# Optimization experiments

Hardware: AMD Instinct MI355X
Metric: run time of the kernel (lower is better)

## Reference

```python
import jax, jax.numpy as jnp
import numpy as np
import math

S, B, D = 2048, 8, 256
HEADS = 8
DPROJ = 128
DFF = 1024
DH = DPROJ // HEADS  # 16


def _layernorm(x, g, b, eps=1e-5):
    mu = jnp.mean(x, axis=-1, keepdims=True)
    var = jnp.mean((x - mu) ** 2, axis=-1, keepdims=True)
    return (x - mu) * jax.lax.rsqrt(var + eps) * g + b


def setup_inputs() -> dict:
    key = jax.random.key(0)
    ks = jax.random.split(key, 16)
    s = 0.02
    return {
        "src": jax.random.normal(ks[0], (S, B, D), dtype=jnp.float32),
        "Wq": jax.random.normal(ks[1], (D, DPROJ), dtype=jnp.float32) * s,
        "bq": jnp.zeros((DPROJ,), dtype=jnp.float32),
        "Wk": jax.random.normal(ks[2], (D, DPROJ), dtype=jnp.float32) * s,
        "bk": jnp.zeros((DPROJ,), dtype=jnp.float32),
        "Wv": jax.random.normal(ks[3], (D, DPROJ), dtype=jnp.float32) * s,
        "bv": jnp.zeros((DPROJ,), dtype=jnp.float32),
        "Wo": jax.random.normal(ks[4], (DPROJ, D), dtype=jnp.float32) * s,
        "ln1_g": jnp.ones((D,), dtype=jnp.float32),
        "ln1_b": jnp.zeros((D,), dtype=jnp.float32),
        "W1": jax.random.normal(ks[5], (D, DFF), dtype=jnp.float32) * s,
        "b1": jnp.zeros((DFF,), dtype=jnp.float32),
        "W2": jax.random.normal(ks[6], (DFF, D), dtype=jnp.float32) * s,
        "b2": jnp.zeros((D,), dtype=jnp.float32),
        "ln2_g": jnp.ones((D,), dtype=jnp.float32),
        "ln2_b": jnp.zeros((D,), dtype=jnp.float32),
    }


def reference(src, Wq, bq, Wk, bk, Wv, bv, Wo, ln1_g, ln1_b, W1, b1, W2, b2, ln2_g, ln2_b):
    # src: (S, B, D)
    q = src @ Wq + bq  # (S, B, DPROJ)
    k = src @ Wk + bk
    v = src @ Wv + bv

    # _reshape_to_batches: (S, B, h*dh) -> (S, B*h, dh), then sdpa moves batch first
    def split_heads(x):
        return jnp.transpose(x.reshape(S, B * HEADS, DH), (1, 0, 2))  # (B*h, S, dh)

    qh, kh, vh = split_heads(q), split_heads(k), split_heads(v)
    scores = jnp.einsum('bid,bjd->bij', qh, kh) / math.sqrt(DH)  # (B*h, S, S)
    attn = jax.nn.softmax(scores, axis=-1)
    ctx = jnp.einsum('bij,bjd->bid', attn, vh)  # (B*h, S, dh)

    # _reshape_from_batches: (B*h, S, dh) -> (S, B, DPROJ)
    ctx = jnp.transpose(ctx, (1, 0, 2)).reshape(S, B, DPROJ)
    y = ctx @ Wo  # (S, B, D), no bias

    x = _layernorm(src + y, ln1_g, ln1_b)
    ffn = jax.nn.relu(x @ W1 + b1) @ W2 + b2
    return _layernorm(x + ffn, ln2_g, ln2_b)
```

## Files before the change

### kernel.cpp

```cpp
#include <hip/hip_runtime.h>
#include <math.h>

#define SLEN 2048
#define BATCH 8
#define DMODEL 256
#define HEADS 8
#define DPROJ 128
#define DFF 1024
#define DH 16
#define MROWS (SLEN*BATCH)

typedef unsigned short u16;
typedef unsigned int u32;
typedef __attribute__((ext_vector_type(8))) short short8;
typedef __attribute__((ext_vector_type(4))) float f32x4;
typedef __attribute__((ext_vector_type(16))) float f32x16;
typedef __attribute__((ext_vector_type(4))) unsigned short u16x4;

__device__ __forceinline__ u16 f2bf(float x) {
    union { float f; u32 u; } v; v.f = x;
    u32 r = v.u + 0x7FFFu + ((v.u >> 16) & 1u);
    return (u16)(r >> 16);
}
__device__ __forceinline__ float bf2f(u16 h) {
    union { u32 u; float f; } v; v.u = ((u32)h) << 16;
    return v.f;
}
__device__ __forceinline__ float fexp2(float x) { return __builtin_amdgcn_exp2f(x); }
__device__ __forceinline__ u32 pack_bf(float lo, float hi) {
    union { float f; u32 u; } a, b; a.f = lo; b.f = hi;
    return __builtin_amdgcn_perm(b.u, a.u, 0x07060302u);
}
__device__ __forceinline__ void gld16(const u16* g, u16* l) {
    __builtin_amdgcn_global_load_lds(
        (const __attribute__((address_space(1))) void*)g,
        (__attribute__((address_space(3))) void*)l, 16, 0, 0);
}

__global__ void prep_kernel(const float* __restrict__ src, u16* __restrict__ srcb,
                            const float* __restrict__ Wq, const float* __restrict__ Wk,
                            const float* __restrict__ Wv, const float* __restrict__ Wo,
                            const float* __restrict__ W1, const float* __restrict__ W2,
                            u16* __restrict__ WqT, u16* __restrict__ WkT,
                            u16* __restrict__ WvT, u16* __restrict__ WoT,
                            u16* __restrict__ W1T, u16* __restrict__ W2T) {
    if (blockIdx.x < 4096) {
        int idx = (blockIdx.x * 256 + threadIdx.x) * 4;
        float4 v = *(const float4*)(src + idx);
        u16x4 o;
        o.x = f2bf(v.x); o.y = f2bf(v.y); o.z = f2bf(v.z); o.w = f2bf(v.w);
        *(u16x4*)(srcb + idx) = o;
        return;
    }
    int i = (blockIdx.x - 4096) * 256 + threadIdx.x;
    if (i < 32768) {
        int n = i >> 8, k = i & 255;
        WqT[i] = f2bf(Wq[k * 128 + n]);
    } else if (i < 65536) {
        int j = i - 32768; int n = j >> 8, k = j & 255;
        WkT[j] = f2bf(Wk[k * 128 + n]);
    } else if (i < 98304) {
        int j = i - 65536; int n = j >> 8, k = j & 255;
        WvT[j] = f2bf(Wv[k * 128 + n]);
    } else if (i < 131072) {
        int j = i - 98304; int n = j >> 7, k = j & 127;
        WoT[j] = f2bf(Wo[k * 256 + n]);
    } else if (i < 393216) {
        int j = i - 131072; int n = j >> 8, k = j & 255;
        W1T[j] = f2bf(W1[k * 1024 + n]);
    } else if (i < 655360) {
        int j = i - 393216; int n = j >> 10, k = j & 1023;
        W2T[j] = f2bf(W2[k * 256 + n]);
    }
}

template<int BN, bool RELU, bool HAS_BIAS, bool OUT_BF16>
__global__ void mfma_gemm(const u16* __restrict__ A, const u16* __restrict__ BT,
                          const float* __restrict__ bias, void* __restrict__ Cout,
                          int M, int N, int K) {
    constexpr int NJ = BN / 32;
    __shared__ __align__(16) u16 As[128 * 32];
    __shared__ __align__(16) u16 Bs[BN * 32];
    const int tid = threadIdx.x;
    const int row0 = blockIdx.x * 128;
    const int col0 = blockIdx.y * BN;
    const int w = tid >> 6, l = tid & 63;
    const int wr = (w & 1) * 64, wc = (w >> 1) * (BN / 2);
    const int lcol = l & 15, lrow = (l >> 4) * 4, g = l >> 4;
    const int sl = l >> 2;
    const int swc = ((l & 3) ^ (sl & 3)) * 8;
    const int fsw = (g ^ (lcol & 3)) * 8;

    const u16* Ag0 = A + (size_t)(row0 + 16 * w + sl) * K + swc;
    const u16* Ag1 = Ag0 + (size_t)64 * K;
    const u16* Bg0 = BT + (size_t)(col0 + 16 * w + sl) * K + swc;
    const u16* Bg1 = Bg0 + (size_t)64 * K;
    u16* lA0 = As + (16 * w) * 32;
    u16* lA1 = As + (16 * w + 64) * 32;
    u16* lB0 = Bs + (16 * w) * 32;
    u16* lB1 = Bs + (16 * w + 64) * 32;

    f32x4 acc[4][NJ] = {};
    for (int k0 = 0; k0 < K; k0 += 32) {
        gld16(Ag0 + k0, lA0);
        gld16(Ag1 + k0, lA1);
        gld16(Bg0 + k0, lB0);
        if (BN == 128) gld16(Bg1 + k0, lB1);
        __syncthreads();
        short8 af[4], bf[NJ];
        #pragma unroll
        for (int i = 0; i < 4; ++i)
            af[i] = *(const short8*)(As + (wr + i * 16 + lcol) * 32 + fsw);
        #pragma unroll
        for (int j = 0; j < NJ; ++j)
            bf[j] = *(const short8*)(Bs + (wc + j * 16 + lcol) * 32 + fsw);
        #pragma unroll
        for (int i = 0; i < 4; ++i)
            #pragma unroll
            for (int j = 0; j < NJ; ++j)
                acc[i][j] = __builtin_amdgcn_mfma_f32_16x16x32_bf16(
                    af[i], bf[j], acc[i][j], 0, 0, 0);
        __syncthreads();
    }
    float bv[NJ];
    #pragma unroll
    for (int j = 0; j < NJ; ++j)
        bv[j] = HAS_BIAS ? bias[col0 + wc + j * 16 + lcol] : 0.f;
    #pragma unroll
    for (int i = 0; i < 4; ++i) {
        #pragma unroll
        for (int r = 0; r < 4; ++r) {
            size_t grow = row0 + wr + i * 16 + lrow + r;
            #pragma unroll
            for (int j = 0; j < NJ; ++j) {
                int gcol = col0 + wc + j * 16 + lcol;
                float c = acc[i][j][r] + bv[j];
                if (RELU) c = fmaxf(c, 0.f);
                if (OUT_BF16) ((u16*)Cout)[grow * N + gcol] = f2bf(c);
                else          ((float*)Cout)[grow * N + gcol] = c;
            }
        }
    }
}

__global__ void qkv_mfma(const u16* __restrict__ A,
                         const u16* __restrict__ WqT, const u16* __restrict__ WkT,
                         const u16* __restrict__ WvT,
                         const float* __restrict__ bq, const float* __restrict__ bk,
                         const float* __restrict__ bv,
                         u16* __restrict__ qhp, u16* __restrict__ khp,
                         u16* __restrict__ vhb) {
    const int which = blockIdx.z;
    const u16* BT   = which == 0 ? WqT : (which == 1 ? WkT : WvT);
    const float* bs = which == 0 ? bq : (which == 1 ? bk : bv);
    u16* outp       = which == 0 ? qhp : (which == 1 ? khp : vhb);
    const float scale = which == 0 ? 0.25f * 1.44269504f : 1.0f;
    __shared__ __align__(16) u16 As[128 * 32];
    __shared__ __align__(16) u16 Bs[128 * 32];
    const int tid = threadIdx.x;
    const int row0 = blockIdx.x * 128;
    const int w = tid >> 6, l = tid & 63;
    const int wr = (w & 1) * 64, wc = (w >> 1) * 64;
    const int lcol = l & 15, lrow = (l >> 4) * 4, g = l >> 4;
    const int sl = l >> 2;
    const int swc = ((l & 3) ^ (sl & 3)) * 8;
    const int fsw = (g ^ (lcol & 3)) * 8;

    const u16* Ag0 = A + (size_t)(row0 + 16 * w + sl) * DMODEL + swc;
    const u16* Ag1 = Ag0 + (size_t)64 * DMODEL;
    const u16* Bg0 = BT + (size_t)(16 * w + sl) * DMODEL + swc;
    const u16* Bg1 = Bg0 + (size_t)64 * DMODEL;
    u16* lA0 = As + (16 * w) * 32;
    u16* lA1 = As + (16 * w + 64) * 32;
    u16* lB0 = Bs + (16 * w) * 32;
    u16* lB1 = Bs + (16 * w + 64) * 32;

    f32x4 acc[4][4] = {};
    for (int k0 = 0; k0 < DMODEL; k0 += 32) {
        gld16(Ag0 + k0, lA0);
        gld16(Ag1 + k0, lA1);
        gld16(Bg0 + k0, lB0);
        gld16(Bg1 + k0, lB1);
        __syncthreads();
        short8 af[4], bf[4];
        #pragma unroll
        for (int i = 0; i < 4; ++i)
            af[i] = *(const short8*)(As + (wr + i * 16 + lcol) * 32 + fsw);
        #pragma unroll
        for (int j = 0; j < 4; ++j)
            bf[j] = *(const short8*)(Bs + (wc + j * 16 + lcol) * 32 + fsw);
        #pragma unroll
        for (int i = 0; i < 4; ++i)
            #pragma unroll
            for (int j = 0; j < 4; ++j)
                acc[i][j] = __builtin_amdgcn_mfma_f32_16x16x32_bf16(
                    af[i], bf[j], acc[i][j], 0, 0, 0);
        __syncthreads();
    }
    #pragma unroll
    for (int i = 0; i < 4; ++i) {
        #pragma unroll
        for (int r = 0; r < 4; ++r) {
            int grow = row0 + wr + i * 16 + lrow + r;
            int b = grow & 7, s = grow >> 3;
            #pragma unroll
            for (int j = 0; j < 4; ++j) {
                int gcol = wc + j * 16 + lcol;
                int h = gcol >> 4, d = gcol & 15;
                float c = acc[i][j][r] + bs[gcol];
                outp[((size_t)(b * 8 + h) * SLEN + s) * 16 + d] = f2bf(c * scale);
            }
        }
    }
}

__global__ void transpose_v(const u16* __restrict__ vhb, u16* __restrict__ va) {
    __shared__ u16 T[128 * 24];
    const int bh = blockIdx.y;
    const int c0 = blockIdx.x * 128;
    const int t = threadIdx.x;
    {
        int key = t >> 1, half = t & 1;
        *(uint4*)(T + key * 24 + half * 8) =
            *(const uint4*)(vhb + ((size_t)bh * SLEN + c0 + key) * 16 + half * 8);
    }
    __syncthreads();
    int d = t >> 4, k8 = (t & 15) * 8;
    u16x4 o0, o1;
    o0.x = T[(k8 + 0) * 24 + d]; o0.y = T[(k8 + 1) * 24 + d];
    o0.z = T[(k8 + 2) * 24 + d]; o0.w = T[(k8 + 3) * 24 + d];
    o1.x = T[(k8 + 4) * 24 + d]; o1.y = T[(k8 + 5) * 24 + d];
    o1.z = T[(k8 + 6) * 24 + d]; o1.w = T[(k8 + 7) * 24 + d];
    u16* dst = va + ((size_t)bh * 32 + d) * SLEN + c0 + k8;
    *(u16x4*)dst = o0;
    *(u16x4*)(dst + 4) = o1;
    if (t < 16) {
        u16x4 ones = { (u16)0x3F80, (u16)0x3F80, (u16)0x3F80, (u16)0x3F80 };
        u16* od = va + ((size_t)bh * 32 + 16) * SLEN + c0 + t * 8;
        *(u16x4*)od = ones;
        *(u16x4*)(od + 4) = ones;
    }
}

__global__ __launch_bounds__(256, 4)
void attn_mfma(const u16* __restrict__ qg, const u16* __restrict__ kg,
               const u16* __restrict__ va, u16* __restrict__ ctx) {
    __shared__ __align__(16) u16 Ps[4 * 2 * 32 * 72];
    const int bh = blockIdx.y;
    const int q0 = blockIdx.x * 128;
    const int tid = threadIdx.x;
    const int w = tid >> 6, l = tid & 63;
    const int n = l & 31, h5 = l >> 5;
    u16* Pbase = Ps + w * (2 * 32 * 72);

    const short8 qf = *(const short8*)(
        qg + ((size_t)bh * SLEN + q0 + w * 32 + n) * 16 + h5 * 8);
    const u16* kb = kg + (size_t)bh * SLEN * 16;
    const u16* vb = va + ((size_t)bh * 32 + n) * SLEN + h5 * 8;

    f32x16 oacc = {};

    short8 kf0 = *(const short8*)(kb + (size_t)n * 16 + h5 * 8);
    short8 kf1 = *(const short8*)(kb + (size_t)(32 + n) * 16 + h5 * 8);

    for (int kt = 0; kt < 32; ++kt) {
        const int k0 = kt * 64;
        u16* Pw = Pbase + (kt & 1) * (32 * 72);
        short8 vf[4];
        #pragma unroll
        for (int st = 0; st < 4; ++st)
            vf[st] = *(const short8*)(vb + k0 + st * 16);
        f32x16 z = {};
        f32x16 s0 = __builtin_amdgcn_mfma_f32_32x32x16_bf16(kf0, qf, z, 0, 0, 0);
        f32x16 s1 = __builtin_amdgcn_mfma_f32_32x32x16_bf16(kf1, qf, z, 0, 0, 0);
        const int kn = (kt < 31) ? (k0 + 64) : 0;
        kf0 = *(const short8*)(kb + (size_t)(kn + n) * 16 + h5 * 8);
        kf1 = *(const short8*)(kb + (size_t)(kn + 32 + n) * 16 + h5 * 8);
        #pragma unroll
        for (int r4 = 0; r4 < 4; ++r4) {
            uint2 d0, d1;
            d0.x = pack_bf(fexp2(s0[r4 * 4 + 0]), fexp2(s0[r4 * 4 + 1]));
            d0.y = pack_bf(fexp2(s0[r4 * 4 + 2]), fexp2(s0[r4 * 4 + 3]));
            d1.x = pack_bf(fexp2(s1[r4 * 4 + 0]), fexp2(s1[r4 * 4 + 1]));
            d1.y = pack_bf(fexp2(s1[r4 * 4 + 2]), fexp2(s1[r4 * 4 + 3]));
            int kbase = 8 * r4 + 4 * h5;
            *(uint2*)(Pw + n * 72 + kbase) = d0;
            *(uint2*)(Pw + n * 72 + 32 + kbase) = d1;
        }
        #pragma unroll
        for (int st = 0; st < 4; ++st) {
            short8 ap = *(const short8*)(Pw + n * 72 + st * 16 + h5 * 8);
            oacc = __builtin_amdgcn_mfma_f32_32x32x16_bf16(ap, vf[st], oacc, 0, 0, 0);
        }
    }
    float* Ob = (float*)Pbase;
    #pragma unroll
    for (int r = 0; r < 16; ++r) {
        int q = (r & 3) + 8 * (r >> 2) + 4 * h5;
        if (n <= 16) Ob[q * 36 + n] = oacc[r];
    }
    __syncthreads();
    const int q = l >> 1, half = l & 1;
    f32x4 o0 = *(const f32x4*)(Ob + q * 36 + half * 8);
    f32x4 o1 = *(const f32x4*)(Ob + q * 36 + half * 8 + 4);
    float rcpL = 1.0f / Ob[q * 36 + 16];
    u16x4 pa, pb;
    pa.x = f2bf(o0[0] * rcpL); pa.y = f2bf(o0[1] * rcpL);
    pa.z = f2bf(o0[2] * rcpL); pa.w = f2bf(o0[3] * rcpL);
    pb.x = f2bf(o1[0] * rcpL); pb.y = f2bf(o1[1] * rcpL);
    pb.z = f2bf(o1[2] * rcpL); pb.w = f2bf(o1[3] * rcpL);
    const int b = bh >> 3, h = bh & 7;
    const int qrow = q0 + w * 32 + q;
    u16* dst = ctx + ((size_t)qrow * BATCH + b) * DPROJ + h * DH + half * 8;
    *(u16x4*)dst = pa;
    *(u16x4*)(dst + 4) = pb;
}

__global__ void ln1_kernel(const float* __restrict__ src, const u16* __restrict__ y,
                           const float* __restrict__ g, const float* __restrict__ bb,
                           u16* __restrict__ xb) {
    const int w = threadIdx.x >> 6, l = threadIdx.x & 63;
    const int row = blockIdx.x * 4 + w;
    const int c = l * 4;
    size_t base = (size_t)row * DMODEL;
    float4 s4 = *(const float4*)(src + base + c);
    u16x4 y4 = *(const u16x4*)(y + base + c);
    float v[4] = { s4.x + bf2f(y4.x), s4.y + bf2f(y4.y),
                   s4.z + bf2f(y4.z), s4.w + bf2f(y4.w) };
    float sum = v[0] + v[1] + v[2] + v[3];
    float ss  = v[0]*v[0] + v[1]*v[1] + v[2]*v[2] + v[3]*v[3];
    #pragma unroll
    for (int off = 1; off < 64; off <<= 1) {
        sum += __shfl_xor(sum, off);
        ss  += __shfl_xor(ss, off);
    }
    float mu = sum * (1.0f / 256.0f);
    float var = ss * (1.0f / 256.0f) - mu * mu;
    float rs = rsqrtf(var + 1e-5f);
    float4 g4 = *(const float4*)(g + c);
    float4 b4 = *(const float4*)(bb + c);
    u16x4 o;
    o.x = f2bf((v[0] - mu) * rs * g4.x + b4.x);
    o.y = f2bf((v[1] - mu) * rs * g4.y + b4.y);
    o.z = f2bf((v[2] - mu) * rs * g4.z + b4.z);
    o.w = f2bf((v[3] - mu) * rs * g4.w + b4.w);
    *(u16x4*)(xb + base + c) = o;
}

__global__ void ln2_kernel(const u16* __restrict__ x, const u16* __restrict__ f,
                           const float* __restrict__ g, const float* __restrict__ bb,
                           float* __restrict__ out) {
    const int w = threadIdx.x >> 6, l = threadIdx.x & 63;
    const int row = blockIdx.x * 4 + w;
    const int c = l * 4;
    size_t base = (size_t)row * DMODEL;
    u16x4 x4 = *(const u16x4*)(x + base + c);
    u16x4 f4 = *(const u16x4*)(f + base + c);
    float v[4] = { bf2f(x4.x) + bf2f(f4.x), bf2f(x4.y) + bf2f(f4.y),
                   bf2f(x4.z) + bf2f(f4.z), bf2f(x4.w) + bf2f(f4.w) };
    float sum = v[0] + v[1] + v[2] + v[3];
    float ss  = v[0]*v[0] + v[1]*v[1] + v[2]*v[2] + v[3]*v[3];
    #pragma unroll
    for (int off = 1; off < 64; off <<= 1) {
        sum += __shfl_xor(sum, off);
        ss  += __shfl_xor(ss, off);
    }
    float mu = sum * (1.0f / 256.0f);
    float var = ss * (1.0f / 256.0f) - mu * mu;
    float rs = rsqrtf(var + 1e-5f);
    float4 g4 = *(const float4*)(g + c);
    float4 b4 = *(const float4*)(bb + c);
    float4 o;
    o.x = (v[0] - mu) * rs * g4.x + b4.x;
    o.y = (v[1] - mu) * rs * g4.y + b4.y;
    o.z = (v[2] - mu) * rs * g4.z + b4.z;
    o.w = (v[3] - mu) * rs * g4.w + b4.w;
    *(float4*)(out + base + c) = o;
}

extern "C" void kernel_launch(void* const* d_in, const int* in_sizes, int n_in,
                              void* d_out, int out_size, void* d_ws, size_t ws_size,
                              hipStream_t stream) {
    const float* src = (const float*)d_in[0];
    const float* Wq  = (const float*)d_in[1];
    const float* bq  = (const float*)d_in[2];
    const float* Wk  = (const float*)d_in[3];
    const float* bk  = (const float*)d_in[4];
    const float* Wv  = (const float*)d_in[5];
    const float* bv  = (const float*)d_in[6];
    const float* Wo  = (const float*)d_in[7];
    const float* g1  = (const float*)d_in[8];
    const float* be1 = (const float*)d_in[9];
    const float* W1  = (const float*)d_in[10];
    const float* b1  = (const float*)d_in[11];
    const float* W2  = (const float*)d_in[12];
    const float* b2  = (const float*)d_in[13];
    const float* g2  = (const float*)d_in[14];
    const float* be2 = (const float*)d_in[15];
    char* ws = (char*)d_ws;
    float* out = (float*)d_out;

    u16* qhp  = (u16*)(ws + 0);
    u16* khp  = (u16*)(ws + 4194304);
    u16* vhb  = (u16*)(ws + 8388608);
    u16* vaug = (u16*)(ws + 12582912);
    u16* ctxb = (u16*)(ws + 20971520);
    u16* yb   = (u16*)(ws + 25165824);
    u16* hb   = (u16*)(ws + 0);
    u16* xb   = (u16*)(ws + 33554432);
    u16* fb   = (u16*)(ws + 41943040);
    u16* srcb = (u16*)(ws + 50331648);
    u16* WqT  = (u16*)(ws + 58720256);
    u16* WkT  = (u16*)(ws + 58785792);
    u16* WvT  = (u16*)(ws + 58851328);
    u16* WoT  = (u16*)(ws + 58916864);
    u16* W1T  = (u16*)(ws + 58982400);
    u16* W2T  = (u16*)(ws + 59506688);

    prep_kernel<<<6656, 256, 0, stream>>>(src, srcb, Wq, Wk, Wv, Wo, W1, W2,
                                          WqT, WkT, WvT, WoT, W1T, W2T);
    qkv_mfma<<<dim3(128, 1, 3), 256, 0, stream>>>(srcb, WqT, WkT, WvT,
                                                  bq, bk, bv, qhp, khp, vhb);
    transpose_v<<<dim3(16, 64), 256, 0, stream>>>(vhb, vaug);
    attn_mfma<<<dim3(16, 64), 256, 0, stream>>>(qhp, khp, vaug, ctxb);
    mfma_gemm<64, false, false, true><<<dim3(128, 4), 256, 0, stream>>>(
        ctxb, WoT, nullptr, yb, MROWS, DMODEL, DPROJ);
    ln1_kernel<<<MROWS / 4, 256, 0, stream>>>(src, yb, g1, be1, xb);
    mfma_gemm<128, true, true, true><<<dim3(128, 8), 256, 0, stream>>>(
        xb, W1T, b1, hb, MROWS, DFF, DMODEL);
    mfma_gemm<64, false, true, true><<<dim3(128, 4), 256, 0, stream>>>(
        hb, W2T, b2, fb, MROWS, DMODEL, DFF);
    ln2_kernel<<<MROWS / 4, 256, 0, stream>>>(xb, fb, g2, be2, out);
}
```

Baseline: 240.4 us.

## Fuse V transpose into QKV epilogue, shrink attention blocks, use bf16 src in LN1

The QKV kernel now writes V directly in the transposed, augmented layout. This removes the separate transpose_v kernel and its intermediate buffer, and the ones row is filled by the prep kernel instead. The attention kernel moves to 128-thread blocks with a single P buffer per wave, padding 68 instead of 72, and register double-buffered prefetch of both K and V fragments for the next tile. LN1 reads the bf16 copy of src instead of fp32, which halves that read traffic but slightly lowers the precision of the residual.

```diff
diff --git a/kernel.cpp b/kernel.cpp
--- a/kernel.cpp
+++ b/kernel.cpp
@@ -43,7 +43,8 @@
                             const float* __restrict__ W1, const float* __restrict__ W2,
                             u16* __restrict__ WqT, u16* __restrict__ WkT,
                             u16* __restrict__ WvT, u16* __restrict__ WoT,
-                            u16* __restrict__ W1T, u16* __restrict__ W2T) {
+                            u16* __restrict__ W1T, u16* __restrict__ W2T,
+                            u16* __restrict__ va) {
     if (blockIdx.x < 4096) {
         int idx = (blockIdx.x * 256 + threadIdx.x) * 4;
         float4 v = *(const float4*)(src + idx);
@@ -71,6 +72,9 @@
     } else if (i < 655360) {
         int j = i - 393216; int n = j >> 10, k = j & 1023;
         W2T[j] = f2bf(W2[k * 256 + n]);
+    } else if (i < 786432) {
+        int j = i - 655360; int bh = j >> 11, col = j & 2047;
+        va[(size_t)bh * 65536 + 16 * 2048 + col] = (u16)0x3F80;
     }
 }
 
@@ -149,11 +153,10 @@
                          const float* __restrict__ bq, const float* __restrict__ bk,
                          const float* __restrict__ bv,
                          u16* __restrict__ qhp, u16* __restrict__ khp,
-                         u16* __restrict__ vhb) {
+                         u16* __restrict__ va) {
     const int which = blockIdx.z;
     const u16* BT   = which == 0 ? WqT : (which == 1 ? WkT : WvT);
     const float* bs = which == 0 ? bq : (which == 1 ? bk : bv);
-    u16* outp       = which == 0 ? qhp : (which == 1 ? khp : vhb);
     const float scale = which == 0 ? 0.25f * 1.44269504f : 1.0f;
     __shared__ __align__(16) u16 As[128 * 32];
     __shared__ __align__(16) u16 Bs[128 * 32];
@@ -208,125 +211,115 @@
                 int gcol = wc + j * 16 + lcol;
                 int h = gcol >> 4, d = gcol & 15;
                 float c = acc[i][j][r] + bs[gcol];
-                outp[((size_t)(b * 8 + h) * SLEN + s) * 16 + d] = f2bf(c * scale);
+                if (which == 2) {
+                    va[((size_t)(b * 8 + h) * 32 + d) * SLEN + s] = f2bf(c);
+                } else {
+                    u16* outp = which == 0 ? qhp : khp;
+                    outp[((size_t)(b * 8 + h) * SLEN + s) * 16 + d] = f2bf(c * scale);
+                }
             }
         }
     }
 }
 
-__global__ void transpose_v(const u16* __restrict__ vhb, u16* __restrict__ va) {
-    __shared__ u16 T[128 * 24];
-    const int bh = blockIdx.y;
-    const int c0 = blockIdx.x * 128;
-    const int t = threadIdx.x;
-    {
-        int key = t >> 1, half = t & 1;
-        *(uint4*)(T + key * 24 + half * 8) =
-            *(const uint4*)(vhb + ((size_t)bh * SLEN + c0 + key) * 16 + half * 8);
-    }
-    __syncthreads();
-    int d = t >> 4, k8 = (t & 15) * 8;
-    u16x4 o0, o1;
-    o0.x = T[(k8 + 0) * 24 + d]; o0.y = T[(k8 + 1) * 24 + d];
-    o0.z = T[(k8 + 2) * 24 + d]; o0.w = T[(k8 + 3) * 24 + d];
-    o1.x = T[(k8 + 4) * 24 + d]; o1.y = T[(k8 + 5) * 24 + d];
-    o1.z = T[(k8 + 6) * 24 + d]; o1.w = T[(k8 + 7) * 24 + d];
-    u16* dst = va + ((size_t)bh * 32 + d) * SLEN + c0 + k8;
-    *(u16x4*)dst = o0;
-    *(u16x4*)(dst + 4) = o1;
-    if (t < 16) {
-        u16x4 ones = { (u16)0x3F80, (u16)0x3F80, (u16)0x3F80, (u16)0x3F80 };
-        u16* od = va + ((size_t)bh * 32 + 16) * SLEN + c0 + t * 8;
-        *(u16x4*)od = ones;
-        *(u16x4*)(od + 4) = ones;
-    }
-}
-
-__global__ __launch_bounds__(256, 4)
+__global__ __launch_bounds__(128, 4)
 void attn_mfma(const u16* __restrict__ qg, const u16* __restrict__ kg,
                const u16* __restrict__ va, u16* __restrict__ ctx) {
-    __shared__ __align__(16) u16 Ps[4 * 2 * 32 * 72];
+    __shared__ __align__(16) u16 Ps[2 * 32 * 68];
     const int bh = blockIdx.y;
-    const int q0 = blockIdx.x * 128;
     const int tid = threadIdx.x;
     const int w = tid >> 6, l = tid & 63;
     const int n = l & 31, h5 = l >> 5;
-    u16* Pbase = Ps + w * (2 * 32 * 72);
-
+    u16* Pw = Ps + w * (32 * 68);
+
+    const int qbase = blockIdx.x * 64 + w * 32;
     const short8 qf = *(const short8*)(
-        qg + ((size_t)bh * SLEN + q0 + w * 32 + n) * 16 + h5 * 8);
+        qg + ((size_t)bh * SLEN + qbase + n) * 16 + h5 * 8);
     const u16* kb = kg + (size_t)bh * SLEN * 16;
     const u16* vb = va + ((size_t)bh * 32 + n) * SLEN + h5 * 8;
 
     f32x16 oacc = {};
-
     short8 kf0 = *(const short8*)(kb + (size_t)n * 16 + h5 * 8);
     short8 kf1 = *(const short8*)(kb + (size_t)(32 + n) * 16 + h5 * 8);
+    short8 vf[4];
+    #pragma unroll
+    for (int st = 0; st < 4; ++st)
+        vf[st] = *(const short8*)(vb + st * 16);
 
     for (int kt = 0; kt < 32; ++kt) {
         const int k0 = kt * 64;
-        u16* Pw = Pbase + (kt & 1) * (32 * 72);
-        short8 vf[4];
-        #pragma unroll
-        for (int st = 0; st < 4; ++st)
-            vf[st] = *(const short8*)(vb + k0 + st * 16);
         f32x16 z = {};
         f32x16 s0 = __builtin_amdgcn_mfma_f32_32x32x16_bf16(kf0, qf, z, 0, 0, 0);
         f32x16 s1 = __builtin_amdgcn_mfma_f32_32x32x16_bf16(kf1, qf, z, 0, 0, 0);
-        const int kn = (kt < 31) ? (k0 + 64) : 0;
-        kf0 = *(const short8*)(kb + (size_t)(kn + n) * 16 + h5 * 8);
-        kf1 = *(const short8*)(kb + (size_t)(kn + 32 + n) * 16 + h5 * 8);
+        const int kn = (k0 + 64) & (SLEN - 1);
+        short8 kf0n = *(const short8*)(kb + (size_t)(kn + n) * 16 + h5 * 8);
+        short8 kf1n = *(const short8*)(kb + (size_t)(kn + 32 + n) * 16 + h5 * 8);
+        short8 vfn[4];
+        #pragma unroll
+        for (int st = 0; st < 4; ++st)
+            vfn[st] = *(const short8*)(vb + kn + st * 16);
         #pragma unroll
         for (int r4 = 0; r4 < 4; ++r4) {
-            uint2 d0, d1;
-            d0.x = pack_bf(fexp2(s0[r4 * 4 + 0]), fexp2(s0[r4 * 4 + 1]));
-            d0.y = pack_bf(fexp2(s0[r4 * 4 + 2]), fexp2(s0[r4 * 4 + 3]));
-            d1.x = pack_bf(fexp2(s1[r4 * 4 + 0]), fexp2(s1[r4 * 4 + 1]));
-            d1.y = pack_bf(fexp2(s1[r4 * 4 + 2]), fexp2(s1[r4 * 4 + 3]));
-            int kbase = 8 * r4 + 4 * h5;
-            *(uint2*)(Pw + n * 72 + kbase) = d0;
-            *(uint2*)(Pw + n * 72 + 32 + kbase) = d1;
+            uint2 d;
+            d.x = pack_bf(fexp2(s0[r4 * 4 + 0]), fexp2(s0[r4 * 4 + 1]));
+            d.y = pack_bf(fexp2(s0[r4 * 4 + 2]), fexp2(s0[r4 * 4 + 3]));
+            *(uint2*)(Pw + n * 68 + 8 * r4 + 4 * h5) = d;
+        }
+        #pragma unroll
+        for (int r4 = 0; r4 < 4; ++r4) {
+            uint2 d;
+            d.x = pack_bf(fexp2(s1[r4 * 4 + 0]), fexp2(s1[r4 * 4 + 1]));
+            d.y = pack_bf(fexp2(s1[r4 * 4 + 2]), fexp2(s1[r4 * 4 + 3]));
+            *(uint2*)(Pw + n * 68 + 32 + 8 * r4 + 4 * h5) = d;
         }
         #pragma unroll
         for (int st = 0; st < 4; ++st) {
-            short8 ap = *(const short8*)(Pw + n * 72 + st * 16 + h5 * 8);
-            oacc = __builtin_amdgcn_mfma_f32_32x32x16_bf16(ap, vf[st], oacc, 0, 0, 0);
-        }
-    }
-    float* Ob = (float*)Pbase;
-    #pragma unroll
-    for (int r = 0; r < 16; ++r) {
-        int q = (r & 3) + 8 * (r >> 2) + 4 * h5;
-        if (n <= 16) Ob[q * 36 + n] = oacc[r];
+            const u16* rp = Pw + n * 68 + st * 16 + h5 * 8;
+            union { uint2 q2[2]; short8 v; } ap;
+            ap.q2[0] = *(const uint2*)rp;
+            ap.q2[1] = *(const uint2*)(rp + 4);
+            oacc = __builtin_amdgcn_mfma_f32_32x32x16_bf16(ap.v, vf[st], oacc, 0, 0, 0);
+        }
+        kf0 = kf0n; kf1 = kf1n;
+        #pragma unroll
+        for (int st = 0; st < 4; ++st) vf[st] = vfn[st];
+    }
+    float* Ob = (float*)Pw;
+    if (n <= 16) {
+        #pragma unroll
+        for (int r = 0; r < 16; ++r) {
+            int qq = (r & 3) + 8 * (r >> 2) + 4 * h5;
+            Ob[qq * 20 + n] = oacc[r];
+        }
     }
     __syncthreads();
     const int q = l >> 1, half = l & 1;
-    f32x4 o0 = *(const f32x4*)(Ob + q * 36 + half * 8);
-    f32x4 o1 = *(const f32x4*)(Ob + q * 36 + half * 8 + 4);
-    float rcpL = 1.0f / Ob[q * 36 + 16];
-    u16x4 pa, pb;
-    pa.x = f2bf(o0[0] * rcpL); pa.y = f2bf(o0[1] * rcpL);
-    pa.z = f2bf(o0[2] * rcpL); pa.w = f2bf(o0[3] * rcpL);
-    pb.x = f2bf(o1[0] * rcpL); pb.y = f2bf(o1[1] * rcpL);
-    pb.z = f2bf(o1[2] * rcpL); pb.w = f2bf(o1[3] * rcpL);
+    f32x4 o0 = *(const f32x4*)(Ob + q * 20 + half * 8);
+    f32x4 o1 = *(const f32x4*)(Ob + q * 20 + half * 8 + 4);
+    float rcp = 1.0f / Ob[q * 20 + 16];
+    u16x4 p0, p1;
+    p0.x = f2bf(o0[0] * rcp); p0.y = f2bf(o0[1] * rcp);
+    p0.z = f2bf(o0[2] * rcp); p0.w = f2bf(o0[3] * rcp);
+    p1.x = f2bf(o1[0] * rcp); p1.y = f2bf(o1[1] * rcp);
+    p1.z = f2bf(o1[2] * rcp); p1.w = f2bf(o1[3] * rcp);
     const int b = bh >> 3, h = bh & 7;
-    const int qrow = q0 + w * 32 + q;
+    const int qrow = qbase + q;
     u16* dst = ctx + ((size_t)qrow * BATCH + b) * DPROJ + h * DH + half * 8;
-    *(u16x4*)dst = pa;
-    *(u16x4*)(dst + 4) = pb;
-}
-
-__global__ void ln1_kernel(const float* __restrict__ src, const u16* __restrict__ y,
+    *(u16x4*)dst = p0;
+    *(u16x4*)(dst + 4) = p1;
+}
+
+__global__ void ln1_kernel(const u16* __restrict__ srcb, const u16* __restrict__ y,
                            const float* __restrict__ g, const float* __restrict__ bb,
                            u16* __restrict__ xb) {
     const int w = threadIdx.x >> 6, l = threadIdx.x & 63;
     const int row = blockIdx.x * 4 + w;
     const int c = l * 4;
     size_t base = (size_t)row * DMODEL;
-    float4 s4 = *(const float4*)(src + base + c);
+    u16x4 s4 = *(const u16x4*)(srcb + base + c);
     u16x4 y4 = *(const u16x4*)(y + base + c);
-    float v[4] = { s4.x + bf2f(y4.x), s4.y + bf2f(y4.y),
-                   s4.z + bf2f(y4.z), s4.w + bf2f(y4.w) };
+    float v[4] = { bf2f(s4.x) + bf2f(y4.x), bf2f(s4.y) + bf2f(y4.y),
+                   bf2f(s4.z) + bf2f(y4.z), bf2f(s4.w) + bf2f(y4.w) };
     float sum = v[0] + v[1] + v[2] + v[3];
     float ss  = v[0]*v[0] + v[1]*v[1] + v[2]*v[2] + v[3]*v[3];
     #pragma unroll
@@ -402,10 +395,9 @@
 
     u16* qhp  = (u16*)(ws + 0);
     u16* khp  = (u16*)(ws + 4194304);
-    u16* vhb  = (u16*)(ws + 8388608);
-    u16* vaug = (u16*)(ws + 12582912);
-    u16* ctxb = (u16*)(ws + 20971520);
-    u16* yb   = (u16*)(ws + 25165824);
+    u16* vaug = (u16*)(ws + 8388608);
+    u16* ctxb = (u16*)(ws + 16777216);
+    u16* yb   = (u16*)(ws + 20971520);
     u16* hb   = (u16*)(ws + 0);
     u16* xb   = (u16*)(ws + 33554432);
     u16* fb   = (u16*)(ws + 41943040);
@@ -417,15 +409,14 @@
     u16* W1T  = (u16*)(ws + 58982400);
     u16* W2T  = (u16*)(ws + 59506688);
 
-    prep_kernel<<<6656, 256, 0, stream>>>(src, srcb, Wq, Wk, Wv, Wo, W1, W2,
-                                          WqT, WkT, WvT, WoT, W1T, W2T);
+    prep_kernel<<<7168, 256, 0, stream>>>(src, srcb, Wq, Wk, Wv, Wo, W1, W2,
+                                          WqT, WkT, WvT, WoT, W1T, W2T, vaug);
     qkv_mfma<<<dim3(128, 1, 3), 256, 0, stream>>>(srcb, WqT, WkT, WvT,
-                                                  bq, bk, bv, qhp, khp, vhb);
-    transpose_v<<<dim3(16, 64), 256, 0, stream>>>(vhb, vaug);
-    attn_mfma<<<dim3(16, 64), 256, 0, stream>>>(qhp, khp, vaug, ctxb);
+                                                  bq, bk, bv, qhp, khp, vaug);
+    attn_mfma<<<dim3(32, 64), 128, 0, stream>>>(qhp, khp, vaug, ctxb);
     mfma_gemm<64, false, false, true><<<dim3(128, 4), 256, 0, stream>>>(
         ctxb, WoT, nullptr, yb, MROWS, DMODEL, DPROJ);
-    ln1_kernel<<<MROWS / 4, 256, 0, stream>>>(src, yb, g1, be1, xb);
+    ln1_kernel<<<MROWS / 4, 256, 0, stream>>>(srcb, yb, g1, be1, xb);
     mfma_gemm<128, true, true, true><<<dim3(128, 8), 256, 0, stream>>>(
         xb, W1T, b1, hb, MROWS, DFF, DMODEL);
     mfma_gemm<64, false, true, true><<<dim3(128, 4), 256, 0, stream>>>(
```

Measured after the change: 240.6 us. About the same (+0.1%).
